# Performance work log

Hardware: AMD Instinct MI355X
Metric: run time of the kernel (lower is better)

## Reference

```python
import jax, jax.numpy as jnp
import numpy as np

# --- static configuration (from init_kwargs / chosen original_size) ---
IMG = 1024            # PromptGetter image_size
DS = 64               # PromptGetter downsizing
ORIG_H, ORIG_W = 1080, 1920
SCALE = IMG / max(ORIG_H, ORIG_W)                 # ResizeLongestSide scale
PRE_H = int(np.floor(ORIG_H * SCALE + 0.5))       # get_prepadded_size -> 576
PRE_W = int(np.floor(ORIG_W * SCALE + 0.5))       # -> 1024
NW = int(ORIG_W * SCALE) // DS                    # grid columns (n_w)
NUM_GRIDS = (IMG // DS) ** 2                      # safe upper bound on grid ids (256)
DEFAULT_THR_TARGET = 0.65
NUM_BG = 1
NUM_LABELS = 16


def setup_inputs() -> dict:
    key = jax.random.key(0)
    k1, k2 = jax.random.split(key)
    return {
        "image_embeddings": jax.random.normal(k1, (1, 256, 64, 64), dtype=jnp.float32),
        "reference_feats": jax.random.normal(k2, (NUM_LABELS, 1, 256), dtype=jnp.float32),
        "original_size": jnp.array([ORIG_H, ORIG_W], dtype=jnp.int32),
        "threshold": jnp.zeros((1, 1), dtype=jnp.float32),  # 0 -> default_threshold_target
        "num_bg_points": 1,
    }


def _postprocess(sim):
    """SAM postprocess_masks: 64x64 -> IMGxIMG -> crop prepadded -> original size."""
    m = jax.image.resize(sim, (IMG, IMG), method="linear")  # align_corners=False bilinear
    m = m[:PRE_H, :PRE_W]
    return jax.image.resize(m, (ORIG_H, ORIG_W), method="linear")


def _point_selection(mask_sim, thr):
    h, w = mask_sim.shape
    flat = mask_sim.reshape(-1)

    # background: k lowest-similarity points (topk largest=False)
    _, bg_idx = jax.lax.top_k(-flat, NUM_BG)
    bg_row = bg_idx // w
    bg_col = bg_idx - bg_row * w
    bg_coords = jnp.stack([bg_col, bg_row], axis=-1).astype(jnp.float32)  # (NUM_BG, 2) as (x, y)

    # foreground: per-grid-cell best-scoring point above threshold.
    # The original gathers torch.where(mask_sim > thr) points and picks the max
    # score per downsized grid cell; here we keep fixed shapes by masking and
    # doing a segment-max over all pixels (same selected points/scores).
    idx = jnp.arange(h * w)
    ys = idx // w
    xs = idx % w
    valid = flat > thr
    grid = ((jnp.floor(ys * SCALE / DS)) * NW + jnp.floor(xs * SCALE / DS)).astype(jnp.int32)
    score = jnp.where(valid, flat, -jnp.inf)
    best = jax.ops.segment_max(score, grid, num_segments=NUM_GRIDS)
    is_best = valid & (flat == best[grid])
    cand = jnp.where(is_best, idx, h * w)
    best_idx = jax.ops.segment_min(cand, grid, num_segments=NUM_GRIDS)  # first max, like torch.topk(k=1)
    grid_ok = jnp.isfinite(best) & (best_idx < h * w)
    safe_idx = jnp.minimum(best_idx, h * w - 1)
    bx = jnp.where(grid_ok, (safe_idx % w).astype(jnp.float32), 0.0)
    by = jnp.where(grid_ok, (safe_idx // w).astype(jnp.float32), 0.0)
    sc = jnp.where(grid_ok, best, -jnp.inf)
    pts = jnp.stack([bx, by, sc], axis=-1)  # (NUM_GRIDS, 3) = (x, y, score)

    # sort by score, descending (empty grid cells sink to the end with -inf)
    order = jnp.argsort(-pts[:, -1])
    return pts[order], bg_coords


def reference(image_embeddings, reference_feats, original_size, threshold, num_bg_points):
    tf = image_embeddings[0]                                   # (C, H, W)
    tf = tf / jnp.linalg.norm(tf, axis=0, keepdims=True)       # channelwise L2 normalize
    c = tf.shape[0]
    tf = tf.reshape(c, -1)                                     # (C, HW)
    thr = ((threshold == 0).astype(threshold.dtype) * DEFAULT_THR_TARGET + threshold)[0, 0]

    def per_label(ref_feat):                                   # ref_feat (1, C)
        sim = (ref_feat @ tf).reshape(64, 64)                  # cosine sim map
        return _point_selection(_postprocess(sim), thr)

    points_scores, bg_coords = jax.vmap(per_label)(reference_feats)
    return points_scores, bg_coords
```

## Files before the change

kernel.cpp:

```cpp
#include <hip/hip_runtime.h>
#include <cmath>
#include <climits>

#define NLAB 16
#define GRIDS 144
#define HOUT 1080
#define WOUT 1920
#define KS2 0.53333336f
#define KS1 0.0625f
#define NEG_MARK -1.0e30f
#define POS_BIG   1.0e30f

__device__ __forceinline__ void taps64(int i, int& t0, int& t1, float& g) {
    float s = ((float)i + 0.5f) * KS1 - 0.5f;
    float f = floorf(s);
    g = s - f;
    int j = (int)f;
    t0 = j < 0 ? 0 : j;
    t1 = j + 1; if (t1 > 63) t1 = 63;
}

__device__ __forceinline__ void fused_taps(int P, int n1m1, int& base,
                                           float& w0, float& w1, float& w2) {
    float sx = ((float)P + 0.5f) * KS2 - 0.5f;
    float fx = floorf(sx);
    float bx = sx - fx;
    int tx = (int)fx;
    int i0 = tx < 0 ? 0 : tx;
    int i1 = tx + 1; if (i1 > n1m1) i1 = n1m1;
    int a0, a1; float ga; taps64(i0, a0, a1, ga);
    int b0, b1; float gb; taps64(i1, b0, b1, gb);
    base = a0;
    w0 = (1.f - bx) * (1.f - ga); w1 = 0.f; w2 = 0.f;
    float c1 = (1.f - bx) * ga;
    if (a1 == base) w0 += c1; else w1 += c1;
    float c2 = bx * (1.f - gb);
    { int o = b0 - base; if (o == 0) w0 += c2; else if (o == 1) w1 += c2; else w2 += c2; }
    float c3 = bx * gb;
    { int o = b1 - base; if (o == 0) w0 += c3; else if (o == 1) w1 += c3; else w2 += c3; }
}

__launch_bounds__(256)
__global__ void sim_kernel(const float* __restrict__ emb,
                           const float* __restrict__ ref,
                           float* __restrict__ sim) {
    __shared__ float rlds[NLAB * 256];
    __shared__ float red[16][NLAB][16];
    __shared__ float n2red[16][16];
    int tid = threadIdx.x;
    for (int i = tid; i < NLAB * 256; i += 256) rlds[i] = ref[i];
    __syncthreads();
    int posl = tid & 15;
    int chunk = tid >> 4;
    int p = blockIdx.x * 16 + posl;
    float acc[NLAB];
#pragma unroll
    for (int l = 0; l < NLAB; ++l) acc[l] = 0.f;
    float n2 = 0.f;
    int cbase = chunk * 16;
#pragma unroll
    for (int cc = 0; cc < 16; ++cc) {
        int c = cbase + cc;
        float v = emb[c * 4096 + p];
        n2 = fmaf(v, v, n2);
#pragma unroll
        for (int l = 0; l < NLAB; ++l)
            acc[l] = fmaf(rlds[l * 256 + c], v, acc[l]);
    }
#pragma unroll
    for (int l = 0; l < NLAB; ++l) red[posl][l][chunk] = acc[l];
    n2red[posl][chunk] = n2;
    __syncthreads();
    int l = chunk;
    float dot = 0.f, nn = 0.f;
#pragma unroll
    for (int k = 0; k < 16; ++k) { dot += red[posl][l][k]; nn += n2red[posl][k]; }
    sim[l * 4096 + p] = dot / sqrtf(nn);
}

__launch_bounds__(256)
__global__ void eval_kernel(const float* __restrict__ simAll,
                            const float* __restrict__ thrPtr,
                            float* __restrict__ gVal, int* __restrict__ gIdx,
                            float* __restrict__ mVal, int* __restrict__ mIdx) {
    int label = blockIdx.x / GRIDS;
    int g = blockIdx.x - label * GRIDS;
    int gy = g >> 4, gx = g & 15;
    int tid = threadIdx.x;

    __shared__ float s8[8][9];
    __shared__ float4 wxT[120];
    __shared__ float rv[4], rmv[4];
    __shared__ int   ri[4], rmi[4];

    int X0 = gx * 120, Y0 = gy * 120;
    int r0, c0; float dw0, dw1, dw2;
    fused_taps(Y0, 575, r0, dw0, dw1, dw2);
    fused_taps(X0, 1023, c0, dw0, dw1, dw2);

    if (tid < 64) {
        int j = tid >> 3, k = tid & 7;
        int rr = r0 + j; if (rr > 63) rr = 63;
        int kk = c0 + k; if (kk > 63) kk = 63;
        s8[j][k] = simAll[label * 4096 + rr * 64 + kk];
    }
    if (tid < 120) {
        int kb; float w0, w1, w2;
        fused_taps(X0 + tid, 1023, kb, w0, w1, w2);
        wxT[tid] = make_float4(w0, w1, w2, __int_as_float(kb - c0));
    }
    __syncthreads();

    float t0v = thrPtr[0];
    float thr = (t0v == 0.0f) ? 0.65f : t0v;

    float bmax = NEG_MARK; int bidx = INT_MAX;
    float vmin = POS_BIG;  int vidx = INT_MAX;

    if (tid < 240) {
        int r = tid >> 1, h = tid & 1;
        int Y = Y0 + r;
        int rb; float wy0, wy1, wy2;
        fused_taps(Y, 575, rb, wy0, wy1, wy2);
        int rl = rb - r0;
        const float* s0 = &s8[rl][0];
        const float* s1 = &s8[rl + 1][0];
        const float* s2 = &s8[rl + 2][0];
        int lx = h * 60;
        int idx = Y * WOUT + X0 + lx;
        int kcur = -1;
        float c0v = 0.f, c1v = 0.f, c2v = 0.f;
#pragma unroll 4
        for (int it = 0; it < 60; ++it) {
            float4 e = wxT[lx];
            int kb = __float_as_int(e.w);
            if (kb != kcur) {
                kcur = kb;
                c0v = fmaf(wy2, s2[kb],     fmaf(wy1, s1[kb],     wy0 * s0[kb]));
                c1v = fmaf(wy2, s2[kb + 1], fmaf(wy1, s1[kb + 1], wy0 * s0[kb + 1]));
                c2v = fmaf(wy2, s2[kb + 2], fmaf(wy1, s1[kb + 2], wy0 * s0[kb + 2]));
            }
            float val = fmaf(e.z, c2v, fmaf(e.y, c1v, e.x * c0v));
            if (val > thr && val > bmax) { bmax = val; bidx = idx; }
            if (val < vmin) { vmin = val; vidx = idx; }
            ++idx; ++lx;
        }
    }

    for (int off = 32; off; off >>= 1) {
        float ov = __shfl_xor(bmax, off); int oi = __shfl_xor(bidx, off);
        if (ov > bmax || (ov == bmax && oi < bidx)) { bmax = ov; bidx = oi; }
        float mv2 = __shfl_xor(vmin, off); int mi2 = __shfl_xor(vidx, off);
        if (mv2 < vmin || (mv2 == vmin && mi2 < vidx)) { vmin = mv2; vidx = mi2; }
    }
    int wave = tid >> 6;
    if ((tid & 63) == 0) { rv[wave] = bmax; ri[wave] = bidx; rmv[wave] = vmin; rmi[wave] = vidx; }
    __syncthreads();
    if (tid == 0) {
#pragma unroll
        for (int w = 1; w < 4; ++w) {
            float ov = rv[w]; int oi = ri[w];
            if (ov > rv[0] || (ov == rv[0] && oi < ri[0])) { rv[0] = ov; ri[0] = oi; }
            float mv2 = rmv[w]; int mi2 = rmi[w];
            if (mv2 < rmv[0] || (mv2 == rmv[0] && mi2 < rmi[0])) { rmv[0] = mv2; rmi[0] = mi2; }
        }
        int o = label * GRIDS + g;
        gVal[o] = rv[0]; gIdx[o] = ri[0];
        mVal[o] = rmv[0]; mIdx[o] = rmi[0];
    }
}

__launch_bounds__(256)
__global__ void final_kernel(const float* __restrict__ gVal, const int* __restrict__ gIdx,
                             const float* __restrict__ mVal, const int* __restrict__ mIdx,
                             float* __restrict__ out) {
    int l = blockIdx.x;
    int tid = threadIdx.x;
    __shared__ float sc[256]; __shared__ int sg[256];
    __shared__ float lx[256], ly[256];

    float score = NEG_MARK;
    float x = 0.0f, y = 0.0f;
    if (tid < GRIDS) {
        float v = gVal[l * GRIDS + tid];
        int i = gIdx[l * GRIDS + tid];
        if (v != NEG_MARK && i < HOUT * WOUT) {
            score = v;
            x = (float)(i % WOUT);
            y = (float)(i / WOUT);
        }
    }
    sc[tid] = score; sg[tid] = tid; lx[tid] = x; ly[tid] = y;
    __syncthreads();

    for (int k = 2; k <= 256; k <<= 1) {
        for (int j = k >> 1; j > 0; j >>= 1) {
            int i2 = tid ^ j;
            if (i2 > tid) {
                float s_a = sc[tid], s_b = sc[i2];
                int g_a = sg[tid], g_b = sg[i2];
                bool up = ((tid & k) == 0);
                bool b_before_a = (s_b > s_a) || (s_b == s_a && g_b < g_a);
                if (b_before_a == up) {
                    sc[tid] = s_b; sc[i2] = s_a;
                    sg[tid] = g_b; sg[i2] = g_a;
                }
            }
            __syncthreads();
        }
    }

    int g2 = sg[tid];
    float* o = out + (l * 256 + tid) * 3;
    o[0] = lx[g2]; o[1] = ly[g2]; o[2] = sc[tid];

    __shared__ float mv[256]; __shared__ int mi[256];
    float v2 = POS_BIG; int i3 = INT_MAX;
    if (tid < GRIDS) { v2 = mVal[l * GRIDS + tid]; i3 = mIdx[l * GRIDS + tid]; }
    mv[tid] = v2; mi[tid] = i3;
    __syncthreads();
    for (int s2 = 128; s2 > 0; s2 >>= 1) {
        if (tid < s2) {
            float ov = mv[tid + s2]; int oi = mi[tid + s2];
            if (ov < mv[tid] || (ov == mv[tid] && oi < mi[tid])) { mv[tid] = ov; mi[tid] = oi; }
        }
        __syncthreads();
    }
    if (tid == 0) {
        int bi = mi[0];
        out[NLAB * 256 * 3 + l * 2 + 0] = (float)(bi % WOUT);
        out[NLAB * 256 * 3 + l * 2 + 1] = (float)(bi / WOUT);
    }
}

extern "C" void kernel_launch(void* const* d_in, const int* in_sizes, int n_in,
                              void* d_out, int out_size, void* d_ws, size_t ws_size,
                              hipStream_t stream) {
    const float* emb = (const float*)d_in[0];
    const float* ref = (const float*)d_in[1];
    const float* thr = (const float*)d_in[3];
    float* out = (float*)d_out;

    float* sim  = (float*)d_ws;
    float* gVal = sim + NLAB * 4096;
    int*   gIdx = (int*)(gVal + NLAB * GRIDS);
    float* mVal = (float*)(gIdx + NLAB * GRIDS);
    int*   mIdx = (int*)(mVal + NLAB * GRIDS);

    sim_kernel<<<256, 256, 0, stream>>>(emb, ref, sim);
    eval_kernel<<<NLAB * GRIDS, 256, 0, stream>>>(sim, thr, gVal, gIdx, mVal, mIdx);
    final_kernel<<<NLAB, 256, 0, stream>>>(gVal, gIdx, mVal, mIdx, out);
}
```

Measured before the change: 91.99 us.

## Fuse final sort into eval kernel via last-block atomic counter

Merges the final per-label sort and background-min reduction into the eval kernel: each block increments a per-label atomic counter, and the last block to finish for a label performs the bitonic sort and writes the outputs. The counters are reset in the sim kernel. The threshold test moves from the per-pixel loop to the per-block result. This removes one kernel launch and its gap, and trims a compare from the inner loop, at the cost of fences and an atomic per block.

```diff
diff --git a/kernel.cpp b/kernel.cpp
--- a/kernel.cpp
+++ b/kernel.cpp
@@ -43,7 +43,9 @@
 __launch_bounds__(256)
 __global__ void sim_kernel(const float* __restrict__ emb,
                            const float* __restrict__ ref,
-                           float* __restrict__ sim) {
+                           float* __restrict__ sim,
+                           int* __restrict__ cnt) {
+    if (blockIdx.x == 0 && threadIdx.x < NLAB) cnt[threadIdx.x] = 0;
     __shared__ float rlds[NLAB * 256];
     __shared__ float red[16][NLAB][16];
     __shared__ float n2red[16][16];
@@ -79,10 +81,12 @@
 }
 
 __launch_bounds__(256)
-__global__ void eval_kernel(const float* __restrict__ simAll,
-                            const float* __restrict__ thrPtr,
-                            float* __restrict__ gVal, int* __restrict__ gIdx,
-                            float* __restrict__ mVal, int* __restrict__ mIdx) {
+__global__ void evalfinal_kernel(const float* __restrict__ simAll,
+                                 const float* __restrict__ thrPtr,
+                                 float* __restrict__ gVal, int* __restrict__ gIdx,
+                                 float* __restrict__ mVal, int* __restrict__ mIdx,
+                                 int* __restrict__ cnt,
+                                 float* __restrict__ out) {
     int label = blockIdx.x / GRIDS;
     int g = blockIdx.x - label * GRIDS;
     int gy = g >> 4, gx = g & 15;
@@ -92,6 +96,7 @@
     __shared__ float4 wxT[120];
     __shared__ float rv[4], rmv[4];
     __shared__ int   ri[4], rmi[4];
+    __shared__ int   lastFlag;
 
     int X0 = gx * 120, Y0 = gy * 120;
     int r0, c0; float dw0, dw1, dw2;
@@ -141,7 +146,7 @@
                 c2v = fmaf(wy2, s2[kb + 2], fmaf(wy1, s1[kb + 2], wy0 * s0[kb + 2]));
             }
             float val = fmaf(e.z, c2v, fmaf(e.y, c1v, e.x * c0v));
-            if (val > thr && val > bmax) { bmax = val; bidx = idx; }
+            if (val > bmax) { bmax = val; bidx = idx; }
             if (val < vmin) { vmin = val; vidx = idx; }
             ++idx; ++lx;
         }
@@ -165,19 +170,20 @@
             if (mv2 < rmv[0] || (mv2 == rmv[0] && mi2 < rmi[0])) { rmv[0] = mv2; rmi[0] = mi2; }
         }
         int o = label * GRIDS + g;
-        gVal[o] = rv[0]; gIdx[o] = ri[0];
+        if (rv[0] > thr) { gVal[o] = rv[0]; gIdx[o] = ri[0]; }
+        else             { gVal[o] = NEG_MARK; gIdx[o] = INT_MAX; }
         mVal[o] = rmv[0]; mIdx[o] = rmi[0];
-    }
-}
-
-__launch_bounds__(256)
-__global__ void final_kernel(const float* __restrict__ gVal, const int* __restrict__ gIdx,
-                             const float* __restrict__ mVal, const int* __restrict__ mIdx,
-                             float* __restrict__ out) {
-    int l = blockIdx.x;
-    int tid = threadIdx.x;
+        __threadfence();
+        int old = atomicAdd(&cnt[label], 1);
+        lastFlag = (old == GRIDS - 1);
+    }
+    __syncthreads();
+    if (!lastFlag) return;
+    __threadfence();
+
+    int l = label;
     __shared__ float sc[256]; __shared__ int sg[256];
-    __shared__ float lx[256], ly[256];
+    __shared__ float lxA[256], lyA[256];
 
     float score = NEG_MARK;
     float x = 0.0f, y = 0.0f;
@@ -190,7 +196,7 @@
             y = (float)(i / WOUT);
         }
     }
-    sc[tid] = score; sg[tid] = tid; lx[tid] = x; ly[tid] = y;
+    sc[tid] = score; sg[tid] = tid; lxA[tid] = x; lyA[tid] = y;
     __syncthreads();
 
     for (int k = 2; k <= 256; k <<= 1) {
@@ -212,22 +218,22 @@
 
     int g2 = sg[tid];
     float* o = out + (l * 256 + tid) * 3;
-    o[0] = lx[g2]; o[1] = ly[g2]; o[2] = sc[tid];
-
-    __shared__ float mv[256]; __shared__ int mi[256];
+    o[0] = lxA[g2]; o[1] = lyA[g2]; o[2] = sc[tid];
+
+    __shared__ float mvS[256]; __shared__ int miS[256];
     float v2 = POS_BIG; int i3 = INT_MAX;
     if (tid < GRIDS) { v2 = mVal[l * GRIDS + tid]; i3 = mIdx[l * GRIDS + tid]; }
-    mv[tid] = v2; mi[tid] = i3;
+    mvS[tid] = v2; miS[tid] = i3;
     __syncthreads();
     for (int s2 = 128; s2 > 0; s2 >>= 1) {
         if (tid < s2) {
-            float ov = mv[tid + s2]; int oi = mi[tid + s2];
-            if (ov < mv[tid] || (ov == mv[tid] && oi < mi[tid])) { mv[tid] = ov; mi[tid] = oi; }
+            float ov = mvS[tid + s2]; int oi = miS[tid + s2];
+            if (ov < mvS[tid] || (ov == mvS[tid] && oi < miS[tid])) { mvS[tid] = ov; miS[tid] = oi; }
         }
         __syncthreads();
     }
     if (tid == 0) {
-        int bi = mi[0];
+        int bi = miS[0];
         out[NLAB * 256 * 3 + l * 2 + 0] = (float)(bi % WOUT);
         out[NLAB * 256 * 3 + l * 2 + 1] = (float)(bi / WOUT);
     }
@@ -246,8 +252,8 @@
     int*   gIdx = (int*)(gVal + NLAB * GRIDS);
     float* mVal = (float*)(gIdx + NLAB * GRIDS);
     int*   mIdx = (int*)(mVal + NLAB * GRIDS);
-
-    sim_kernel<<<256, 256, 0, stream>>>(emb, ref, sim);
-    eval_kernel<<<NLAB * GRIDS, 256, 0, stream>>>(sim, thr, gVal, gIdx, mVal, mIdx);
-    final_kernel<<<NLAB, 256, 0, stream>>>(gVal, gIdx, mVal, mIdx, out);
-}
+    int*   cnt  = (int*)(mIdx + NLAB * GRIDS);
+
+    sim_kernel<<<256, 256, 0, stream>>>(emb, ref, sim, cnt);
+    evalfinal_kernel<<<NLAB * GRIDS, 256, 0, stream>>>(sim, thr, gVal, gIdx, mVal, mIdx, cnt, out);
+}
```

After: 136.3 us. 48.2% more time.
